# Optimization experiments

Hardware: AMD Instinct MI355X
Metric: run time of the kernel (lower is better)

Reference implementation:

```python
import jax, jax.numpy as jnp
import numpy as np

H = 16  # number of heads

def setup_inputs() -> dict:
    key = jax.random.key(0)
    ks = jax.random.split(key, 8)
    B, T, D = 4, 2048, 1024
    s = 0.02
    return {
        "query": jax.random.normal(ks[0], (B, T, D), jnp.float32),
        "key":   jax.random.normal(ks[1], (B, T, D), jnp.float32),
        "value": jax.random.normal(ks[2], (B, T, D), jnp.float32),
        "mask":  jnp.ones((B, T, T), jnp.int32),
        # torch nn.Linear weights: [out_features, in_features]
        "Wq": jax.random.normal(ks[3], (D, D), jnp.float32) * s,
        "Wk": jax.random.normal(ks[4], (D, D), jnp.float32) * s,
        "Wv": jax.random.normal(ks[5], (D, D), jnp.float32) * s,
        "Wo": jax.random.normal(ks[6], (D, D), jnp.float32) * s,
        "bo": jnp.zeros((D,), jnp.float32),
    }

def reference(query, key, value, mask, Wq, Wk, Wv, Wo, bo):
    B, Tq, _ = query.shape
    Tk = key.shape[1]
    Dv = Wv.shape[0]
    # linear projections (y = x @ W^T), split into heads: [B, H, T, dh]
    Q = jnp.einsum('btd,ed->bte', query, Wq).reshape(B, Tq, H, -1).transpose(0, 2, 1, 3)
    K = jnp.einsum('btd,ed->bte', key,   Wk).reshape(B, Tk, H, -1).transpose(0, 2, 1, 3)
    V = jnp.einsum('btd,ed->bte', value, Wv).reshape(B, Tk, H, -1).transpose(0, 2, 1, 3)
    d_k = K.shape[-1]
    scores = jnp.einsum('bhqd,bhkd->bhqk', Q, K) / jnp.sqrt(jnp.asarray(d_k, Q.dtype))
    # mask broadcast: [B,1,Tq,Tk]; masked_fill(mask==0, -1e9)
    scores = jnp.where(mask[:, None] == 0, jnp.asarray(-1e9, scores.dtype), scores)
    attn = jax.nn.softmax(scores, axis=-1)
    Z = jnp.einsum('bhqk,bhkd->bhqd', attn, V)          # [B,H,Tq,dh]
    Zc = Z.transpose(0, 2, 1, 3).reshape(B, Tq, Dv)     # concat heads
    return jnp.einsum('btd,ed->bte', Zc, Wo) + bo
```

## Files before the change

kernel.cpp:

```cpp
#include <hip/hip_runtime.h>

typedef __bf16 bf16x8 __attribute__((ext_vector_type(8)));
typedef float f32x4 __attribute__((ext_vector_type(4)));
typedef unsigned short u16;
typedef unsigned long long u64;

#define NX 8388608
#define NW 1048576

__device__ __forceinline__ u16 f2bf(float f) {
  union { float f; unsigned u; } c; c.f = f;
  unsigned u = c.u;
  u += 0x7fffu + ((u >> 16) & 1u);
  return (u16)(u >> 16);
}

__device__ __forceinline__ f32x4 mfma16(bf16x8 a, bf16x8 b, f32x4 c) {
  return __builtin_amdgcn_mfma_f32_16x16x32_bf16(a, b, c, 0, 0, 0);
}

__device__ __forceinline__ void gld16(void* lds, const void* g) {
  __builtin_amdgcn_global_load_lds(
      (const __attribute__((address_space(1))) unsigned int*)g,
      (__attribute__((address_space(3))) unsigned int*)lds, 16, 0, 0);
}

__global__ __launch_bounds__(256) void cast_all(
    const float* __restrict__ q, const float* __restrict__ k,
    const float* __restrict__ v, const float* __restrict__ wq,
    const float* __restrict__ wk, const float* __restrict__ wv,
    const float* __restrict__ wo, u16* __restrict__ xbf, u16* __restrict__ wbf) {
  long long i = ((long long)blockIdx.x * 256 + threadIdx.x) * 8;
  const float* src; u16* dst; long long off;
  if (i < (long long)NX)            { src = q; dst = xbf;            off = i; }
  else if (i < 2LL * NX)            { src = k; dst = xbf + NX;       off = i - NX; }
  else if (i < 3LL * NX)            { src = v; dst = xbf + 2LL * NX; off = i - 2LL * NX; }
  else {
    long long j = i - 3LL * NX;
    int w = (int)(j / NW); off = j - (long long)w * NW;
    src = (w == 0) ? wq : (w == 1) ? wk : (w == 2) ? wv : wo;
    dst = wbf + (long long)w * NW;
  }
  float4 a = *(const float4*)(src + off);
  float4 b = *(const float4*)(src + off + 4);
  u16 o[8] = {f2bf(a.x), f2bf(a.y), f2bf(a.z), f2bf(a.w),
              f2bf(b.x), f2bf(b.y), f2bf(b.z), f2bf(b.w)};
  *(uint4*)(dst + off) = *(const uint4*)o;
}

__global__ __launch_bounds__(256) void mask_pack(
    const int* __restrict__ mask, u64* __restrict__ bits) {
  const int row = blockIdx.x * 4 + (threadIdx.x >> 6);
  const int lane = threadIdx.x & 63;
  const int* mrow = mask + (long long)row * 2048;
#pragma unroll
  for (int it = 0; it < 32; it++) {
    u64 w = __ballot(mrow[it * 64 + lane] != 0);
    if (lane == 0) bits[row * 32 + it] = w;
  }
}

template <int MODE>
__global__ __launch_bounds__(256, 2) void gemm128(
    const u16* __restrict__ Abase, const u16* __restrict__ Wbase,
    u16* __restrict__ oq, u16* __restrict__ ok, u16* __restrict__ ovt,
    const float* __restrict__ bias, float* __restrict__ of) {
  __shared__ u16 smem[2][128 * 64];
  u16* sA = smem[0];
  u16* sB = smem[1];
  const u16* A = Abase;
  const u16* W = Wbase;
  if (MODE == 0) { A += (long long)blockIdx.z * NX; W += (long long)blockIdx.z * NW; }
  const int tid = threadIdx.x, wave = tid >> 6, lane = tid & 63;
  const int quad = lane >> 4, l15 = lane & 15;
  const int m0 = blockIdx.y * 128, n0 = blockIdx.x * 128;
  const int wm = (wave & 1) * 64, wn = (wave >> 1) * 64;
  const int lr = lane >> 3;
  const int gc = (lane & 7) ^ lr;
  f32x4 acc[4][4];
#pragma unroll
  for (int i = 0; i < 4; i++)
#pragma unroll
    for (int j = 0; j < 4; j++) acc[i][j] = (f32x4){0.f, 0.f, 0.f, 0.f};

  for (int ks = 0; ks < 16; ks++) {
    const int k0 = ks * 64;
    __syncthreads();
#pragma unroll
    for (int t = 0; t < 4; t++) {
      const int rb = wave * 32 + t * 8;
      gld16(&sA[rb * 64], &A[(m0 + rb + lr) * 1024 + k0 + gc * 8]);
      gld16(&sB[rb * 64], &W[(n0 + rb + lr) * 1024 + k0 + gc * 8]);
    }
    __syncthreads();
#pragma unroll
    for (int kc = 0; kc < 2; kc++) {
      bf16x8 aF[4], bF[4];
#pragma unroll
      for (int i = 0; i < 4; i++)
        aF[i] = *(const bf16x8*)&sA[(wm + 16 * i + l15) * 64 +
                                    (((kc * 4 + quad) ^ (l15 & 7)) * 8)];
#pragma unroll
      for (int j = 0; j < 4; j++)
        bF[j] = *(const bf16x8*)&sB[(wn + 16 * j + l15) * 64 +
                                    (((kc * 4 + quad) ^ (l15 & 7)) * 8)];
#pragma unroll
      for (int i = 0; i < 4; i++)
#pragma unroll
        for (int j = 0; j < 4; j++) acc[i][j] = mfma16(aF[i], bF[j], acc[i][j]);
    }
  }

  if (MODE == 0) {
    const int z = blockIdx.z;
    if (z < 2) {
      const float qscale = (z == 0) ? 0.18033688f : 1.0f;
      u16* dst = (z == 0) ? oq : ok;
#pragma unroll
      for (int i = 0; i < 4; i++)
#pragma unroll
        for (int j = 0; j < 4; j++)
#pragma unroll
          for (int r = 0; r < 4; r++) {
            int m = m0 + wm + 16 * i + quad * 4 + r;
            int n = n0 + wn + 16 * j + l15;
            int b = m >> 11, t = m & 2047, h = n >> 6, d = n & 63;
            dst[(((b << 4) + h) * 2048 + t) * 64 + d] = f2bf(acc[i][j][r] * qscale);
          }
    } else {
      __syncthreads();
      u16* sT = &smem[0][0] + wave * 4096;
#pragma unroll
      for (int i = 0; i < 4; i++)
#pragma unroll
        for (int j = 0; j < 4; j++)
#pragma unroll
          for (int r = 0; r < 4; r++) {
            int m = 16 * i + quad * 4 + r;
            int n = 16 * j + l15;
            sT[n * 64 + (((m >> 3) ^ (n & 7)) * 8) + (m & 7)] = f2bf(acc[i][j][r]);
          }
      const int b = m0 >> 11, t0 = (m0 + wm) & 2047;
      const int h = (n0 + wn) >> 6;
      u16* dst = ovt + ((long long)((b << 4) + h)) * 131072 + lane * 2048 + t0;
#pragma unroll
      for (int c = 0; c < 8; c++) {
        uint4 val = *(const uint4*)&sT[lane * 64 + ((c ^ (lane & 7)) * 8)];
        *(uint4*)(dst + c * 8) = val;
      }
    }
  } else {
    float bb[4];
#pragma unroll
    for (int j = 0; j < 4; j++) bb[j] = bias[n0 + wn + 16 * j + l15];
#pragma unroll
    for (int i = 0; i < 4; i++)
#pragma unroll
      for (int j = 0; j < 4; j++)
#pragma unroll
        for (int r = 0; r < 4; r++) {
          int m = m0 + wm + 16 * i + quad * 4 + r;
          int n = n0 + wn + 16 * j + l15;
          of[m * 1024 + n] = acc[i][j][r] + bb[j];
        }
  }
}

__global__ __launch_bounds__(256, 3) void attn(
    const u16* __restrict__ Qh, const u16* __restrict__ Kh,
    const u16* __restrict__ Vt, const u64* __restrict__ mbits,
    u16* __restrict__ Zc) {
  __shared__ u16 sK[128 * 64];
  __shared__ u16 sV[64 * 128];
  __shared__ alignas(16) u16 sP[4][16][136];
  const int tid = threadIdx.x, wave = tid >> 6, lane = tid & 63;
  const int quad = lane >> 4, l15 = lane & 15;
  const int bh = blockIdx.y, b = bh >> 4, h = bh & 15, qt = blockIdx.x;
  const int q0 = qt * 64 + wave * 16;
  const int lr8 = lane >> 3, gc8 = (lane & 7) ^ (lr8 & 7);
  const int lr4 = lane >> 4, lc16 = lane & 15;

  bf16x8 qa[2];
#pragma unroll
  for (int kc = 0; kc < 2; kc++)
    qa[kc] = *(const bf16x8*)&Qh[(bh * 2048 + q0 + l15) * 64 + kc * 32 + quad * 8];

  const u64* mb = mbits + (long long)(b * 2048 + q0 + quad * 4) * 32;

  f32x4 oacc[4];
#pragma unroll
  for (int j = 0; j < 4; j++) oacc[j] = (f32x4){0.f, 0.f, 0.f, 0.f};
  float lv[4] = {0.f, 0.f, 0.f, 0.f};

  for (int kt = 0; kt < 16; kt++) {
    __syncthreads();
#pragma unroll
    for (int t = 0; t < 4; t++) {
      const int rbk = wave * 32 + t * 8;
      const int kap = (((rbk & 15) + lr8) << 3) + (rbk >> 4);
      gld16(&sK[rbk * 64], &Kh[(bh * 2048 + kt * 128 + kap) * 64 + gc8 * 8]);
      const int rbv = wave * 16 + t * 4;
      gld16(&sV[rbv * 128],
            &Vt[(bh * 64 + rbv + lr4) * 2048 + kt * 128 + ((lc16 ^ (t * 4 + lr4)) * 8)]);
    }
    u64 mw[4][2];
#pragma unroll
    for (int r = 0; r < 4; r++) {
      mw[r][0] = mb[r * 32 + 2 * kt];
      mw[r][1] = mb[r * 32 + 2 * kt + 1];
    }
    __syncthreads();

    f32x4 sacc[8];
#pragma unroll
    for (int j = 0; j < 8; j++) sacc[j] = (f32x4){0.f, 0.f, 0.f, 0.f};
#pragma unroll
    for (int kc = 0; kc < 2; kc++)
#pragma unroll
      for (int j = 0; j < 8; j++) {
        bf16x8 kF = *(const bf16x8*)&sK[(16 * j + l15) * 64 +
                                        (((kc * 4 + quad) ^ (l15 & 7)) * 8)];
        sacc[j] = mfma16(qa[kc], kF, sacc[j]);
      }

    bool full = __all((mw[0][0] & mw[0][1] & mw[1][0] & mw[1][1] &
                       mw[2][0] & mw[2][1] & mw[3][0] & mw[3][1]) == ~0ull);
    if (full) {
#pragma unroll
      for (int r = 0; r < 4; r++) {
        bf16x8 pk;
        float ls = 0.f;
#pragma unroll
        for (int j = 0; j < 8; j++) {
          float p = __builtin_amdgcn_exp2f(sacc[j][r]);
          ls += p;
          pk[j] = (__bf16)p;
        }
        lv[r] += ls;
        *(bf16x8*)&sP[wave][quad * 4 + r][l15 * 8] = pk;
      }
    } else {
#pragma unroll
      for (int r = 0; r < 4; r++) {
        bf16x8 pk;
        float ls = 0.f;
        u64 w = mw[r][l15 >> 3];
#pragma unroll
        for (int j = 0; j < 8; j++) {
          float p = __builtin_amdgcn_exp2f(sacc[j][r]);
          p = ((w >> (((l15 & 7) << 3) + j)) & 1ull) ? p : 0.f;
          ls += p;
          pk[j] = (__bf16)p;
        }
        lv[r] += ls;
        *(bf16x8*)&sP[wave][quad * 4 + r][l15 * 8] = pk;
      }
    }

#pragma unroll
    for (int kc = 0; kc < 4; kc++) {
      bf16x8 aP = *(const bf16x8*)&sP[wave][l15][kc * 32 + quad * 8];
#pragma unroll
      for (int j = 0; j < 4; j++) {
        bf16x8 vF = *(const bf16x8*)&sV[(16 * j + l15) * 128 +
                                        (((kc * 4 + quad) ^ l15) * 8)];
        oacc[j] = mfma16(aP, vF, oacc[j]);
      }
    }
  }

  float inv[4];
#pragma unroll
  for (int r = 0; r < 4; r++) {
    float s = lv[r];
    s += __shfl_xor(s, 1);
    s += __shfl_xor(s, 2);
    s += __shfl_xor(s, 4);
    s += __shfl_xor(s, 8);
    inv[r] = 1.f / s;
  }
#pragma unroll
  for (int j = 0; j < 4; j++)
#pragma unroll
    for (int r = 0; r < 4; r++) {
      int t = q0 + quad * 4 + r;
      Zc[(b * 2048 + t) * 1024 + h * 64 + 16 * j + l15] = f2bf(oacc[j][r] * inv[r]);
    }
}

extern "C" void kernel_launch(void* const* d_in, const int* in_sizes, int n_in,
                              void* d_out, int out_size, void* d_ws, size_t ws_size,
                              hipStream_t stream) {
  (void)in_sizes; (void)n_in; (void)out_size; (void)ws_size;
  const float* q    = (const float*)d_in[0];
  const float* k    = (const float*)d_in[1];
  const float* v    = (const float*)d_in[2];
  const int*   mask = (const int*)d_in[3];
  const float* Wq   = (const float*)d_in[4];
  const float* Wk   = (const float*)d_in[5];
  const float* Wv   = (const float*)d_in[6];
  const float* Wo   = (const float*)d_in[7];
  const float* bo   = (const float*)d_in[8];
  float* out = (float*)d_out;

  u16* Xbf = (u16*)d_ws;
  u16* Wbf = Xbf + 3LL * NX;
  u16* Qh  = Wbf + 4LL * NW;
  u16* Kh  = Qh + (long long)NX;
  u16* Vt  = Kh + (long long)NX;
  u16* Zc  = Vt + (long long)NX;
  u64* Mb  = (u64*)(Zc + (long long)NX);

  cast_all<<<14336, 256, 0, stream>>>(q, k, v, Wq, Wk, Wv, Wo, Xbf, Wbf);
  mask_pack<<<2048, 256, 0, stream>>>(mask, Mb);
  gemm128<0><<<dim3(8, 64, 3), 256, 0, stream>>>(Xbf, Wbf, Qh, Kh, Vt, nullptr, nullptr);
  attn<<<dim3(32, 64), 256, 0, stream>>>(Qh, Kh, Vt, Mb, Zc);
  gemm128<1><<<dim3(8, 64), 256, 0, stream>>>(Zc, Wbf + 3LL * NW, nullptr, nullptr, nullptr,
                                              bo, out);
}
```

Measured before the change: 400.2 us.

## Process 32 query rows per wave in attention to reuse K/V tiles

Each attention wave now handles two 16-row query groups (128 queries per block), so every K and V fragment read from LDS feeds two MFMAs, and each loaded K/V tile serves twice as many queries. The grid is halved and launch bounds drop from 3 to 2 blocks per CU to make room for the doubled accumulators and score registers. This halves global K/V traffic and LDS fragment reads per query, at the cost of higher register pressure, lower occupancy and fewer blocks (1024) to spread across CUs.

```diff
diff --git a/kernel.cpp b/kernel.cpp
--- a/kernel.cpp
+++ b/kernel.cpp
@@ -166,31 +166,39 @@
   }
 }
 
-__global__ __launch_bounds__(256, 3) void attn(
+__global__ __launch_bounds__(256, 2) void attn(
     const u16* __restrict__ Qh, const u16* __restrict__ Kh,
     const u16* __restrict__ Vt, const u64* __restrict__ mbits,
     u16* __restrict__ Zc) {
   __shared__ u16 sK[128 * 64];
   __shared__ u16 sV[64 * 128];
-  __shared__ alignas(16) u16 sP[4][16][136];
+  __shared__ alignas(16) u16 sP[4][32][136];
   const int tid = threadIdx.x, wave = tid >> 6, lane = tid & 63;
   const int quad = lane >> 4, l15 = lane & 15;
   const int bh = blockIdx.y, b = bh >> 4, h = bh & 15, qt = blockIdx.x;
-  const int q0 = qt * 64 + wave * 16;
+  const int q0 = qt * 128 + wave * 32;
   const int lr8 = lane >> 3, gc8 = (lane & 7) ^ (lr8 & 7);
   const int lr4 = lane >> 4, lc16 = lane & 15;
 
-  bf16x8 qa[2];
-#pragma unroll
-  for (int kc = 0; kc < 2; kc++)
-    qa[kc] = *(const bf16x8*)&Qh[(bh * 2048 + q0 + l15) * 64 + kc * 32 + quad * 8];
-
-  const u64* mb = mbits + (long long)(b * 2048 + q0 + quad * 4) * 32;
-
-  f32x4 oacc[4];
-#pragma unroll
-  for (int j = 0; j < 4; j++) oacc[j] = (f32x4){0.f, 0.f, 0.f, 0.f};
-  float lv[4] = {0.f, 0.f, 0.f, 0.f};
+  bf16x8 qa[2][2];
+#pragma unroll
+  for (int g = 0; g < 2; g++)
+#pragma unroll
+    for (int kc = 0; kc < 2; kc++)
+      qa[g][kc] = *(const bf16x8*)&Qh[(bh * 2048 + q0 + g * 16 + l15) * 64 +
+                                      kc * 32 + quad * 8];
+
+  const u64* mb[2];
+#pragma unroll
+  for (int g = 0; g < 2; g++)
+    mb[g] = mbits + (long long)(b * 2048 + q0 + g * 16 + quad * 4) * 32;
+
+  f32x4 oacc[2][4];
+#pragma unroll
+  for (int g = 0; g < 2; g++)
+#pragma unroll
+    for (int j = 0; j < 4; j++) oacc[g][j] = (f32x4){0.f, 0.f, 0.f, 0.f};
+  float lv[2][4] = {{0.f, 0.f, 0.f, 0.f}, {0.f, 0.f, 0.f, 0.f}};
 
   for (int kt = 0; kt < 16; kt++) {
     __syncthreads();
@@ -203,89 +211,108 @@
       gld16(&sV[rbv * 128],
             &Vt[(bh * 64 + rbv + lr4) * 2048 + kt * 128 + ((lc16 ^ (t * 4 + lr4)) * 8)]);
     }
-    u64 mw[4][2];
-#pragma unroll
-    for (int r = 0; r < 4; r++) {
-      mw[r][0] = mb[r * 32 + 2 * kt];
-      mw[r][1] = mb[r * 32 + 2 * kt + 1];
-    }
+    u64 mw[2][4][2];
+#pragma unroll
+    for (int g = 0; g < 2; g++)
+#pragma unroll
+      for (int r = 0; r < 4; r++) {
+        mw[g][r][0] = mb[g][r * 32 + 2 * kt];
+        mw[g][r][1] = mb[g][r * 32 + 2 * kt + 1];
+      }
     __syncthreads();
 
-    f32x4 sacc[8];
-#pragma unroll
-    for (int j = 0; j < 8; j++) sacc[j] = (f32x4){0.f, 0.f, 0.f, 0.f};
+    f32x4 sacc[2][8];
+#pragma unroll
+    for (int g = 0; g < 2; g++)
+#pragma unroll
+      for (int j = 0; j < 8; j++) sacc[g][j] = (f32x4){0.f, 0.f, 0.f, 0.f};
 #pragma unroll
     for (int kc = 0; kc < 2; kc++)
 #pragma unroll
       for (int j = 0; j < 8; j++) {
         bf16x8 kF = *(const bf16x8*)&sK[(16 * j + l15) * 64 +
                                         (((kc * 4 + quad) ^ (l15 & 7)) * 8)];
-        sacc[j] = mfma16(qa[kc], kF, sacc[j]);
-      }
-
-    bool full = __all((mw[0][0] & mw[0][1] & mw[1][0] & mw[1][1] &
-                       mw[2][0] & mw[2][1] & mw[3][0] & mw[3][1]) == ~0ull);
+        sacc[0][j] = mfma16(qa[0][kc], kF, sacc[0][j]);
+        sacc[1][j] = mfma16(qa[1][kc], kF, sacc[1][j]);
+      }
+
+    u64 allm = ~0ull;
+#pragma unroll
+    for (int g = 0; g < 2; g++)
+#pragma unroll
+      for (int r = 0; r < 4; r++) allm &= mw[g][r][0] & mw[g][r][1];
+    bool full = __all(allm == ~0ull);
     if (full) {
 #pragma unroll
-      for (int r = 0; r < 4; r++) {
-        bf16x8 pk;
-        float ls = 0.f;
-#pragma unroll
-        for (int j = 0; j < 8; j++) {
-          float p = __builtin_amdgcn_exp2f(sacc[j][r]);
-          ls += p;
-          pk[j] = (__bf16)p;
+      for (int g = 0; g < 2; g++)
+#pragma unroll
+        for (int r = 0; r < 4; r++) {
+          bf16x8 pk;
+          float ls = 0.f;
+#pragma unroll
+          for (int j = 0; j < 8; j++) {
+            float p = __builtin_amdgcn_exp2f(sacc[g][j][r]);
+            ls += p;
+            pk[j] = (__bf16)p;
+          }
+          lv[g][r] += ls;
+          *(bf16x8*)&sP[wave][g * 16 + quad * 4 + r][l15 * 8] = pk;
         }
-        lv[r] += ls;
-        *(bf16x8*)&sP[wave][quad * 4 + r][l15 * 8] = pk;
-      }
     } else {
 #pragma unroll
-      for (int r = 0; r < 4; r++) {
-        bf16x8 pk;
-        float ls = 0.f;
-        u64 w = mw[r][l15 >> 3];
-#pragma unroll
-        for (int j = 0; j < 8; j++) {
-          float p = __builtin_amdgcn_exp2f(sacc[j][r]);
-          p = ((w >> (((l15 & 7) << 3) + j)) & 1ull) ? p : 0.f;
-          ls += p;
-          pk[j] = (__bf16)p;
+      for (int g = 0; g < 2; g++)
+#pragma unroll
+        for (int r = 0; r < 4; r++) {
+          bf16x8 pk;
+          float ls = 0.f;
+          u64 w = mw[g][r][l15 >> 3];
+#pragma unroll
+          for (int j = 0; j < 8; j++) {
+            float p = __builtin_amdgcn_exp2f(sacc[g][j][r]);
+            p = ((w >> (((l15 & 7) << 3) + j)) & 1ull) ? p : 0.f;
+            ls += p;
+            pk[j] = (__bf16)p;
+          }
+          lv[g][r] += ls;
+          *(bf16x8*)&sP[wave][g * 16 + quad * 4 + r][l15 * 8] = pk;
         }
-        lv[r] += ls;
-        *(bf16x8*)&sP[wave][quad * 4 + r][l15 * 8] = pk;
-      }
     }
 
 #pragma unroll
     for (int kc = 0; kc < 4; kc++) {
-      bf16x8 aP = *(const bf16x8*)&sP[wave][l15][kc * 32 + quad * 8];
+      bf16x8 aP0 = *(const bf16x8*)&sP[wave][l15][kc * 32 + quad * 8];
+      bf16x8 aP1 = *(const bf16x8*)&sP[wave][16 + l15][kc * 32 + quad * 8];
 #pragma unroll
       for (int j = 0; j < 4; j++) {
         bf16x8 vF = *(const bf16x8*)&sV[(16 * j + l15) * 128 +
                                         (((kc * 4 + quad) ^ l15) * 8)];
-        oacc[j] = mfma16(aP, vF, oacc[j]);
-      }
-    }
-  }
-
-  float inv[4];
-#pragma unroll
-  for (int r = 0; r < 4; r++) {
-    float s = lv[r];
-    s += __shfl_xor(s, 1);
-    s += __shfl_xor(s, 2);
-    s += __shfl_xor(s, 4);
-    s += __shfl_xor(s, 8);
-    inv[r] = 1.f / s;
-  }
-#pragma unroll
-  for (int j = 0; j < 4; j++)
+        oacc[0][j] = mfma16(aP0, vF, oacc[0][j]);
+        oacc[1][j] = mfma16(aP1, vF, oacc[1][j]);
+      }
+    }
+  }
+
+#pragma unroll
+  for (int g = 0; g < 2; g++) {
+    float inv[4];
 #pragma unroll
     for (int r = 0; r < 4; r++) {
-      int t = q0 + quad * 4 + r;
-      Zc[(b * 2048 + t) * 1024 + h * 64 + 16 * j + l15] = f2bf(oacc[j][r] * inv[r]);
-    }
+      float s = lv[g][r];
+      s += __shfl_xor(s, 1);
+      s += __shfl_xor(s, 2);
+      s += __shfl_xor(s, 4);
+      s += __shfl_xor(s, 8);
+      inv[r] = 1.f / s;
+    }
+#pragma unroll
+    for (int j = 0; j < 4; j++)
+#pragma unroll
+      for (int r = 0; r < 4; r++) {
+        int t = q0 + g * 16 + quad * 4 + r;
+        Zc[(b * 2048 + t) * 1024 + h * 64 + 16 * j + l15] =
+            f2bf(oacc[g][j][r] * inv[r]);
+      }
+  }
 }
 
 extern "C" void kernel_launch(void* const* d_in, const int* in_sizes, int n_in,
@@ -314,7 +341,7 @@
   cast_all<<<14336, 256, 0, stream>>>(q, k, v, Wq, Wk, Wv, Wo, Xbf, Wbf);
   mask_pack<<<2048, 256, 0, stream>>>(mask, Mb);
   gemm128<0><<<dim3(8, 64, 3), 256, 0, stream>>>(Xbf, Wbf, Qh, Kh, Vt, nullptr, nullptr);
-  attn<<<dim3(32, 64), 256, 0, stream>>>(Qh, Kh, Vt, Mb, Zc);
+  attn<<<dim3(16, 64), 256, 0, stream>>>(Qh, Kh, Vt, Mb, Zc);
   gemm128<1><<<dim3(8, 64), 256, 0, stream>>>(Zc, Wbf + 3LL * NW, nullptr, nullptr, nullptr,
                                               bo, out);
 }
```

Measured after the change: 399.1 us. No clear change (-0.3%).
